# Optimization experiments

Measured on AMD Instinct MI355X. Metric: run time of the kernel, lower is better.

The kernel has to match this reference:

```python
import jax, jax.numpy as jnp
import numpy as np
from jax import lax

B, N, T, F, H, R = 32, 1024, 32, 5, 64, 5


def setup_inputs() -> dict:
    key = jax.random.key(0)
    ks = jax.random.split(key, 12)
    sc = 0.1
    x = jax.random.normal(ks[0], (B, N, T, F), dtype=jnp.float32)
    A = jax.random.randint(ks[1], (N, N, R), 0, 2).astype(jnp.float32)
    return {
        "x": x,
        "A": A,
        # nn.LSTM params (torch layout: [4H, in], gate order i,f,g,o)
        "lstm_Wih": jax.random.normal(ks[2], (4 * H, F), dtype=jnp.float32) * sc,
        "lstm_Whh": jax.random.normal(ks[3], (4 * H, H), dtype=jnp.float32) * sc,
        "lstm_bih": jax.random.normal(ks[4], (4 * H,), dtype=jnp.float32) * sc,
        "lstm_bhh": jax.random.normal(ks[5], (4 * H,), dtype=jnp.float32) * sc,
        # attention Linear(H, 1)
        "attn_w": jax.random.normal(ks[6], (1, H), dtype=jnp.float32) * sc,
        "attn_b": jax.random.normal(ks[7], (1,), dtype=jnp.float32) * sc,
        # GNN edge-gate Linear(R, 1)
        "gnn_w": jax.random.normal(ks[8], (1, R), dtype=jnp.float32) * sc,
        "gnn_b": jax.random.normal(ks[9], (1,), dtype=jnp.float32) * sc,
        # pred Linear(2H, 1)
        "pred_w": jax.random.normal(ks[10], (1, 2 * H), dtype=jnp.float32) * sc,
        "pred_b": jax.random.normal(ks[11], (1,), dtype=jnp.float32) * sc,
    }


def _lstm_attn(x, Wih, Whh, bih, bhh, attn_w, attn_b):
    # x: [BN, T, F] -> attended hidden [BN, H]
    BN, Tt, _ = x.shape
    Hh = Whh.shape[1]
    pre = x @ Wih.T + (bih + bhh)  # [BN, T, 4H] input projections precomputed

    def step(carry, xt):
        h, c = carry
        gates = xt + h @ Whh.T
        i, f, g, o = jnp.split(gates, 4, axis=-1)
        c = jax.nn.sigmoid(f) * c + jax.nn.sigmoid(i) * jnp.tanh(g)
        h = jax.nn.sigmoid(o) * jnp.tanh(c)
        return (h, c), h

    init = (jnp.zeros((BN, Hh), x.dtype), jnp.zeros((BN, Hh), x.dtype))
    _, hs = lax.scan(step, init, pre.transpose(1, 0, 2))
    hs = hs.transpose(1, 0, 2)  # [BN, T, H]
    scores = jnp.tanh(hs @ attn_w.T + attn_b)      # [BN, T, 1]
    aw = jax.nn.softmax(scores, axis=1)            # softmax over time
    return jnp.sum(hs * aw, axis=1)                # [BN, H]


def reference(x, A, lstm_Wih, lstm_Whh, lstm_bih, lstm_bhh,
              attn_w, attn_b, gnn_w, gnn_b, pred_w, pred_b):
    Bb, Nn, Tt, Ff = x.shape
    Hh = lstm_Whh.shape[1]
    # LSTM+attention shared across stocks -> fold stocks into batch
    e_old = _lstm_attn(x.reshape(Bb * Nn, Tt, Ff), lstm_Wih, lstm_Whh,
                       lstm_bih, lstm_bhh, attn_w, attn_b).reshape(Bb, Nn, Hh)

    # GNN: per-edge gate w[i,j] = LeakyReLU(Linear(A[i,j,:])), active if sum(A[i,j])>0
    mask = (jnp.sum(A, axis=-1) > 0).astype(e_old.dtype)             # [N, N]
    w = jax.nn.leaky_relu((A @ gnn_w.T + gnn_b)[..., 0], 0.2)        # [N, N]
    deg = jnp.sum(mask, axis=1)                                      # [N] active neighbor count
    coef = mask * w                                                  # [N, N]
    dots = jnp.einsum('bik,bjk->bij', e_old, e_old)                  # [B, N, N]
    e_new = jnp.einsum('bij,ij,bjk->bik', dots, coef, e_old) / deg[None, :, None]
    e_final = jnp.concatenate([e_old, e_new], axis=-1)               # [B, N, 2H]
    preds = e_final @ pred_w.T + pred_b                              # [B, N, 1]
    return preds
```

## Files before the change

### kernel.cpp

```cpp
#include <hip/hip_runtime.h>

constexpr int Bc = 32, Nc = 1024, Tc = 32, Fc = 5, Hc = 64;
constexpr int BNc = Bc * Nc;

#define DEVFN __device__ __forceinline__

typedef _Float16 f16x8 __attribute__((ext_vector_type(8)));
typedef _Float16 f16x4 __attribute__((ext_vector_type(4)));
typedef float    f32x16 __attribute__((ext_vector_type(16)));

DEVFN float fast_rcp(float x) { return __builtin_amdgcn_rcpf(x); }
DEVFN float tanh_fast(float x) { return 1.f - 2.f * fast_rcp(__expf(2.f * x) + 1.f); }

__global__ __launch_bounds__(128, 2) void lstm_attn_kernel(
    const float* __restrict__ x,
    const float* __restrict__ Wih,
    const float* __restrict__ Whh,
    const float* __restrict__ bih,
    const float* __restrict__ bhh,
    const float* __restrict__ attn_w,
    const float* __restrict__ attn_b,
    _Float16* __restrict__ E16,
    _Float16* __restrict__ ET)
{
    constexpr int XP = 164;
    constexpr int HP = 68;
    __shared__ __align__(16) _Float16 xs[32 * XP];
    __shared__ __align__(16) _Float16 hb[2][32 * HP];
    __shared__ float ap[2][32];
    float* es = (float*)xs;

    const int tid  = threadIdx.x;
    const int w    = tid >> 6;
    const int lane = tid & 63;
    const int m    = lane & 31;
    const int hi   = lane >> 5;

    const float* xg = x + (size_t)blockIdx.x * 32 * Tc * Fc;
    for (int i = tid; i < 32 * 160; i += 128) {
        int mm = i / 160, o = i - mm * 160;
        xs[mm * XP + o] = (_Float16)xg[i];
    }
    for (int i = tid; i < 32 * HP / 2; i += 128) ((uint*)&hb[0][0])[i] = 0u;

    f16x8 af[4][5];
    #pragma unroll
    for (int g = 0; g < 4; ++g) {
        const int j = 32 * (2 * g + w) + m;
        #pragma unroll
        for (int kt = 0; kt < 4; ++kt) {
            const float* wp = Whh + j * 64 + kt * 16 + 8 * hi;
            float4 u0 = *(const float4*)wp;
            float4 u1 = *(const float4*)(wp + 4);
            af[g][kt] = f16x8{(_Float16)u0.x, (_Float16)u0.y, (_Float16)u0.z, (_Float16)u0.w,
                              (_Float16)u1.x, (_Float16)u1.y, (_Float16)u1.z, (_Float16)u1.w};
        }
        float v[8];
        #pragma unroll
        for (int e = 0; e < 5; ++e) v[e] = Wih[j * Fc + e];
        v[5] = bih[j] + bhh[j]; v[6] = 0.f; v[7] = 0.f;
        #pragma unroll
        for (int e = 0; e < 8; ++e) {
            float z = hi ? 0.f : v[e];
            af[g][4][e] = (_Float16)z;
        }
    }

    float aw_own[16];
    #pragma unroll
    for (int a2 = 0; a2 < 4; ++a2)
        #pragma unroll
        for (int p = 0; p < 4; ++p)
            aw_own[a2 * 4 + p] = attn_w[32 * w + 8 * a2 + 4 * hi + p];
    const float ab = attn_b[0];

    float hcur[16], cst[16], oacc[16];
    #pragma unroll
    for (int i = 0; i < 16; ++i) { hcur[i] = 0.f; cst[i] = 0.f; oacc[i] = 0.f; }
    float lsum = 0.f;

    f32x16 zero16 = {0,0,0,0,0,0,0,0,0,0,0,0,0,0,0,0};
    const int xrow = m * XP;
    const int swz  = m & 15;
    __syncthreads();

    f16x8 bf[5];
    #pragma unroll
    for (int kt = 0; kt < 4; ++kt) {
        f16x4 lo = *(const f16x4*)&hb[0][m * HP + ((4 * kt + 2 * hi)     ^ swz) * 4];
        f16x4 hh = *(const f16x4*)&hb[0][m * HP + ((4 * kt + 2 * hi + 1) ^ swz) * 4];
        bf[kt] = f16x8{lo[0], lo[1], lo[2], lo[3], hh[0], hh[1], hh[2], hh[3]};
    }
    {
        #pragma unroll
        for (int e = 0; e < 8; ++e) bf[4][e] = (_Float16)0.f;
        if (!hi) {
            #pragma unroll
            for (int e = 0; e < 5; ++e) bf[4][e] = xs[xrow + e];
            bf[4][5] = (_Float16)1.f;
        }
    }

    #pragma unroll 1
    for (int t = 0; t < Tc; ++t) {
        f32x16 acc[4];
        #pragma unroll
        for (int g = 0; g < 4; ++g) {
            acc[g] = __builtin_amdgcn_mfma_f32_32x32x16_f16(af[g][0], bf[0], zero16, 0, 0, 0);
            #pragma unroll
            for (int kt = 1; kt < 5; ++kt)
                acc[g] = __builtin_amdgcn_mfma_f32_32x32x16_f16(af[g][kt], bf[kt], acc[g], 0, 0, 0);
        }
        float attnp = 0.f;
        #pragma unroll
        for (int r = 0; r < 16; ++r) {
            float ei = __expf(-acc[0][r]);
            float ef = __expf(-acc[1][r]);
            float Eg = __expf(2.f * acc[2][r]);
            float eo = __expf(-acc[3][r]);
            float u  = 1.f + ei;
            float v  = 1.f + ef;
            float wq = Eg + 1.f;
            float z  = Eg - 1.f;
            float t1 = u * wq;
            float num = fmaf(cst[r], t1, z * v);
            float cn = num * fast_rcp(t1 * v);
            cst[r] = cn;
            float E2 = __expf(2.f * cn);
            float hv = (E2 - 1.f) * fast_rcp((E2 + 1.f) * (1.f + eo));
            hcur[r] = hv;
            attnp = fmaf(hv, aw_own[r], attnp);
        }
        _Float16* hw = &hb[(t + 1) & 1][0];
        #pragma unroll
        for (int a2 = 0; a2 < 4; ++a2) {
            f16x4 pk = {(_Float16)hcur[4 * a2 + 0], (_Float16)hcur[4 * a2 + 1],
                        (_Float16)hcur[4 * a2 + 2], (_Float16)hcur[4 * a2 + 3]};
            *(f16x4*)&hw[m * HP + ((8 * w + 2 * a2 + hi) ^ swz) * 4] = pk;
        }
        attnp += __shfl_xor(attnp, 32);
        if (!hi) ap[w][m] = attnp;
        __syncthreads();
        float sc = tanh_fast(ap[0][m] + ap[1][m] + ab);
        float ew = __expf(sc);
        lsum += ew;
        #pragma unroll
        for (int i = 0; i < 16; ++i) oacc[i] = fmaf(ew, hcur[i], oacc[i]);
        if (t != Tc - 1) {
            const _Float16* hr = &hb[(t + 1) & 1][0];
            #pragma unroll
            for (int kt = 0; kt < 4; ++kt) {
                f16x4 lo = *(const f16x4*)&hr[m * HP + ((4 * kt + 2 * hi)     ^ swz) * 4];
                f16x4 hh = *(const f16x4*)&hr[m * HP + ((4 * kt + 2 * hi + 1) ^ swz) * 4];
                bf[kt] = f16x8{lo[0], lo[1], lo[2], lo[3], hh[0], hh[1], hh[2], hh[3]};
            }
            if (!hi) {
                #pragma unroll
                for (int e = 0; e < 5; ++e) bf[4][e] = xs[xrow + (t + 1) * Fc + e];
                bf[4][5] = (_Float16)1.f;
            }
        }
    }

    __syncthreads();
    const float li = fast_rcp(lsum);
    #pragma unroll
    for (int r = 0; r < 16; ++r) {
        int u = 32 * w + 8 * (r >> 2) + 4 * hi + (r & 3);
        es[m * 65 + u] = oacc[r] * li;
    }
    __syncthreads();

    uint* E16u = (uint*)E16 + (size_t)blockIdx.x * 32 * 32;
    for (int idx = tid; idx < 32 * 32; idx += 128) {
        int mm = idx >> 5, hp = idx & 31;
        union { _Float16 h2[2]; uint u; } cv;
        cv.h2[0] = (_Float16)es[mm * 65 + 2 * hp];
        cv.h2[1] = (_Float16)es[mm * 65 + 2 * hp + 1];
        E16u[idx] = cv.u;
    }
    const int bb_ = blockIdx.x >> 5, n0d = (blockIdx.x & 31) * 16;
    uint* ETu = (uint*)ET;
    for (int idx = tid; idx < 64 * 16; idx += 128) {
        int h = idx >> 4, c = idx & 15;
        union { _Float16 h2[2]; uint u; } cv;
        cv.h2[0] = (_Float16)es[(2 * c) * 65 + h];
        cv.h2[1] = (_Float16)es[(2 * c + 1) * 65 + h];
        ETu[((size_t)bb_ * 64 + h) * 512 + n0d + c] = cv.u;
    }
}

__global__ __launch_bounds__(256) void coefq_kernel(
    const float* __restrict__ A,
    const float* __restrict__ gnn_w,
    const float* __restrict__ gnn_b,
    float* __restrict__ coefQ,
    float* __restrict__ deg)
{
    __shared__ float ct[64 * 68];
    const int t = threadIdx.x;
    const int it = blockIdx.x >> 4, jt = blockIdx.x & 15;
    const int i_loc = t >> 2, chunk = t & 3;
    float gw[5];
    #pragma unroll
    for (int f = 0; f < 5; ++f) gw[f] = gnn_w[f];
    const float gb = gnn_b[0];

    const float* Ab = A + ((size_t)(it * 64 + i_loc) * 1024 + jt * 64 + chunk * 16) * 5;
    float buf[80];
    #pragma unroll
    for (int k = 0; k < 20; ++k)
        *(float4*)&buf[4 * k] = ((const float4*)Ab)[k];

    float cnt = 0.f;
    #pragma unroll
    for (int jj = 0; jj < 16; ++jj) {
        float s = 0.f, d = gb;
        #pragma unroll
        for (int f = 0; f < 5; ++f) { float vv = buf[5 * jj + f]; s += vv; d = fmaf(vv, gw[f], d); }
        float cf = (s > 0.f) ? (d >= 0.f ? d : 0.2f * d) : 0.f;
        ct[i_loc * 68 + chunk * 16 + jj] = cf;
        cnt += (s > 0.f) ? 1.f : 0.f;
    }
    cnt += __shfl_xor(cnt, 1);
    cnt += __shfl_xor(cnt, 2);
    if ((t & 3) == 0) atomicAdd(&deg[it * 64 + i_loc], cnt);
    __syncthreads();

    const int i_o = t & 63;
    #pragma unroll
    for (int p = 0; p < 4; ++p) {
        int jg = (t >> 6) + 4 * p;
        float4 v = *(const float4*)&ct[i_o * 68 + 4 * jg];
        ((float4*)coefQ)[(size_t)(jt * 16 + jg) * 1024 + it * 64 + i_o] = v;
    }
}

__global__ __launch_bounds__(256, 2) void gnn_pred_kernel(
    const _Float16* __restrict__ E16,
    const _Float16* __restrict__ ET,
    const float* __restrict__ coefQ,
    const float* __restrict__ deg,
    const float* __restrict__ pred_w,
    const float* __restrict__ pred_b,
    float* __restrict__ preds)
{
    __shared__ __align__(16) _Float16 tiles[2][4][64 * 64];
    const int tid  = threadIdx.x;
    const int w    = tid >> 6;
    const int lane = tid & 63;
    const int l31  = lane & 31;
    const int hi   = lane >> 5;
    const int it   = blockIdx.x >> 5;
    const int b    = blockIdx.x & 31;

    _Float16* EA = &tiles[0][w][0];
    _Float16* EB = &tiles[1][w][0];
    const float4* coefQ4 = (const float4*)coefQ;

    f16x8 eb[2][4];
    #pragma unroll
    for (int ni = 0; ni < 2; ++ni)
        #pragma unroll
        for (int kt = 0; kt < 4; ++kt)
            eb[ni][kt] = *(const f16x8*)(E16 +
                ((size_t)(b * 1024 + it * 64 + ni * 32 + l31) * 64 + 16 * kt + 8 * hi));

    f32x16 zero16 = {0,0,0,0,0,0,0,0,0,0,0,0,0,0,0,0};
    f32x16 oacc[2][2];
    #pragma unroll
    for (int mi = 0; mi < 2; ++mi)
        #pragma unroll
        for (int nh = 0; nh < 2; ++nh) oacc[mi][nh] = zero16;

    #pragma unroll 1
    for (int s = 0; s < 4; ++s) {
        const int jt = w * 4 + s;
        const _Float16* srcA = E16 + (size_t)(b * 1024 + jt * 64) * 64;
        const _Float16* srcB = ET + (size_t)b * 64 * 1024 + jt * 64;
        #pragma unroll
        for (int q = 0; q < 8; ++q) {
            int f = q * 64 + lane, r = f >> 3, c = f & 7;
            uint4 va = *(const uint4*)(srcA + r * 64 + c * 8);
            *(uint4*)(EA + r * 64 + ((c ^ (r & 7)) * 8)) = va;
            uint4 vb = *(const uint4*)(srcB + r * 1024 + c * 8);
            *(uint4*)(EB + r * 64 + ((c ^ (r & 7)) * 8)) = vb;
        }
        #pragma unroll 1
        for (int mj = 0; mj < 2; ++mj) {
            f16x8 af[4];
            #pragma unroll
            for (int kt = 0; kt < 4; ++kt)
                af[kt] = *(const f16x8*)(EA + (mj * 32 + l31) * 64 +
                                         (((2 * kt + hi) ^ (l31 & 7)) * 8));
            #pragma unroll
            for (int mi = 0; mi < 2; ++mi) {
                f32x16 a = __builtin_amdgcn_mfma_f32_32x32x16_f16(af[0], eb[mi][0], zero16, 0, 0, 0);
                #pragma unroll
                for (int kt = 1; kt < 4; ++kt)
                    a = __builtin_amdgcn_mfma_f32_32x32x16_f16(af[kt], eb[mi][kt], a, 0, 0, 0);
                #pragma unroll
                for (int rg = 0; rg < 4; ++rg) {
                    int j0 = jt * 64 + mj * 32 + 8 * rg + 4 * hi;
                    float4 cf = coefQ4[(size_t)(j0 >> 2) * 1024 + it * 64 + mi * 32 + l31];
                    a[4 * rg + 0] *= cf.x; a[4 * rg + 1] *= cf.y;
                    a[4 * rg + 2] *= cf.z; a[4 * rg + 3] *= cf.w;
                }
                f16x8 pa[2];
                #pragma unroll
                for (int kk = 0; kk < 2; ++kk) {
                    const int rg = 2 * kk;
                    #pragma unroll
                    for (int c4 = 0; c4 < 4; ++c4) {
                        float own_lo = a[rg * 4 + c4];
                        float own_hi = a[(rg + 1) * 4 + c4];
                        float send = hi ? own_lo : own_hi;
                        float recv = __shfl_xor(send, 32);
                        float lo = hi ? recv : own_lo;
                        float hv = hi ? own_hi : recv;
                        pa[kk][c4]     = (_Float16)lo;
                        pa[kk][4 + c4] = (_Float16)hv;
                    }
                }
                #pragma unroll
                for (int nh = 0; nh < 2; ++nh)
                    #pragma unroll
                    for (int kk = 0; kk < 2; ++kk) {
                        const int ktj = 2 * mj + kk;
                        f16x8 bb = *(const f16x8*)(EB + (nh * 32 + l31) * 64 +
                                                   (((2 * ktj + hi) ^ (l31 & 7)) * 8));
                        oacc[mi][nh] = __builtin_amdgcn_mfma_f32_32x32x16_f16(
                            pa[kk], bb, oacc[mi][nh], 0, 0, 0);
                    }
            }
        }
    }

    const float pwh0 = pred_w[64 + l31];
    const float pwh1 = pred_w[96 + l31];
    #pragma unroll
    for (int mi = 0; mi < 2; ++mi)
        #pragma unroll
        for (int r = 0; r < 16; ++r) {
            float v = oacc[mi][0][r] * pwh0 + oacc[mi][1][r] * pwh1;
            v += __shfl_xor(v, 1);  v += __shfl_xor(v, 2);  v += __shfl_xor(v, 4);
            v += __shfl_xor(v, 8);  v += __shfl_xor(v, 16);
            int i_loc = mi * 32 + 8 * (r >> 2) + (r & 3) + 4 * hi;
            int gi = it * 64 + i_loc;
            if (l31 == 0) {
                float dg = deg[gi];
                atomicAdd(&preds[b * 1024 + gi], v * fast_rcp(dg));
            }
        }
    if (w == 0) {
        const float pb0 = pred_b[0];
        #pragma unroll
        for (int ni = 0; ni < 2; ++ni) {
            float dot = 0.f;
            #pragma unroll
            for (int kt = 0; kt < 4; ++kt)
                #pragma unroll
                for (int e = 0; e < 8; ++e)
                    dot = fmaf((float)eb[ni][kt][e], pred_w[16 * kt + 8 * hi + e], dot);
            dot += __shfl_xor(dot, 32);
            if (hi == 0)
                atomicAdd(&preds[b * 1024 + it * 64 + ni * 32 + l31], dot + pb0);
        }
    }
}

extern "C" void kernel_launch(void* const* d_in, const int* in_sizes, int n_in,
                              void* d_out, int out_size, void* d_ws, size_t ws_size,
                              hipStream_t stream) {
    const float* x      = (const float*)d_in[0];
    const float* A      = (const float*)d_in[1];
    const float* Wih    = (const float*)d_in[2];
    const float* Whh    = (const float*)d_in[3];
    const float* bih    = (const float*)d_in[4];
    const float* bhh    = (const float*)d_in[5];
    const float* attn_w = (const float*)d_in[6];
    const float* attn_b = (const float*)d_in[7];
    const float* gnn_w  = (const float*)d_in[8];
    const float* gnn_b  = (const float*)d_in[9];
    const float* pred_w = (const float*)d_in[10];
    const float* pred_b = (const float*)d_in[11];
    float* preds = (float*)d_out;

    _Float16* E16 = (_Float16*)d_ws;
    _Float16* ET  = E16 + (size_t)BNc * Hc;
    float* coefQ  = (float*)(ET + (size_t)BNc * Hc);
    float* deg    = coefQ + (size_t)Nc * Nc;

    hipMemsetAsync(preds, 0, (size_t)out_size * sizeof(float), stream);
    hipMemsetAsync(deg, 0, Nc * sizeof(float), stream);

    lstm_attn_kernel<<<BNc / 32, 128, 0, stream>>>(x, Wih, Whh, bih, bhh,
                                                   attn_w, attn_b, E16, ET);
    coefq_kernel<<<256, 256, 0, stream>>>(A, gnn_w, gnn_b, coefQ, deg);
    gnn_pred_kernel<<<Bc * (Nc / 64), 256, 0, stream>>>(E16, ET, coefQ, deg,
                                                        pred_w, pred_b, preds);
}
```

Measured before the change: 237.3 us.

## Split LSTM gates across four waves and drop LDS staging in GNN kernel

The LSTM kernel now runs 256 threads per block, with each wave computing two interleaved gate tiles so a lane holds all four gates of a hidden unit. The h exchange uses a single 16-byte swizzled LDS write and read per step instead of split 8-byte accesses. The GNN kernel halves the row tile to 32, reads E16/ET directly from global memory instead of staging them in LDS, and reduces across waves in shared memory so it can write preds directly, removing the atomics and the memset. The goal is more parallelism and occupancy in the latency-bound recurrence, at the cost of more global loads in the GNN stage.

```diff
diff --git a/kernel.cpp b/kernel.cpp
--- a/kernel.cpp
+++ b/kernel.cpp
@@ -6,13 +6,12 @@
 #define DEVFN __device__ __forceinline__
 
 typedef _Float16 f16x8 __attribute__((ext_vector_type(8)));
-typedef _Float16 f16x4 __attribute__((ext_vector_type(4)));
 typedef float    f32x16 __attribute__((ext_vector_type(16)));
 
 DEVFN float fast_rcp(float x) { return __builtin_amdgcn_rcpf(x); }
 DEVFN float tanh_fast(float x) { return 1.f - 2.f * fast_rcp(__expf(2.f * x) + 1.f); }
 
-__global__ __launch_bounds__(128, 2) void lstm_attn_kernel(
+__global__ __launch_bounds__(256, 3) void lstm_attn_kernel(
     const float* __restrict__ x,
     const float* __restrict__ Wih,
     const float* __restrict__ Whh,
@@ -24,10 +23,9 @@
     _Float16* __restrict__ ET)
 {
     constexpr int XP = 164;
-    constexpr int HP = 68;
     __shared__ __align__(16) _Float16 xs[32 * XP];
-    __shared__ __align__(16) _Float16 hb[2][32 * HP];
-    __shared__ float ap[2][32];
+    __shared__ __align__(16) _Float16 hb[2][32 * 64];
+    __shared__ float ap[4][32];
     float* es = (float*)xs;
 
     const int tid  = threadIdx.x;
@@ -37,23 +35,23 @@
     const int hi   = lane >> 5;
 
     const float* xg = x + (size_t)blockIdx.x * 32 * Tc * Fc;
-    for (int i = tid; i < 32 * 160; i += 128) {
+    for (int i = tid; i < 32 * 160; i += 256) {
         int mm = i / 160, o = i - mm * 160;
         xs[mm * XP + o] = (_Float16)xg[i];
     }
-    for (int i = tid; i < 32 * HP / 2; i += 128) ((uint*)&hb[0][0])[i] = 0u;
-
-    f16x8 af[4][5];
-    #pragma unroll
-    for (int g = 0; g < 4; ++g) {
-        const int j = 32 * (2 * g + w) + m;
+
+    f16x8 af[2][5];
+    #pragma unroll
+    for (int tt = 0; tt < 2; ++tt) {
+        const int jt = 2 * w + tt;
+        const int j  = 64 * (m & 3) + 8 * jt + (m >> 2);
         #pragma unroll
         for (int kt = 0; kt < 4; ++kt) {
             const float* wp = Whh + j * 64 + kt * 16 + 8 * hi;
             float4 u0 = *(const float4*)wp;
             float4 u1 = *(const float4*)(wp + 4);
-            af[g][kt] = f16x8{(_Float16)u0.x, (_Float16)u0.y, (_Float16)u0.z, (_Float16)u0.w,
-                              (_Float16)u1.x, (_Float16)u1.y, (_Float16)u1.z, (_Float16)u1.w};
+            af[tt][kt] = f16x8{(_Float16)u0.x, (_Float16)u0.y, (_Float16)u0.z, (_Float16)u0.w,
+                               (_Float16)u1.x, (_Float16)u1.y, (_Float16)u1.z, (_Float16)u1.w};
         }
         float v[8];
         #pragma unroll
@@ -62,98 +60,102 @@
         #pragma unroll
         for (int e = 0; e < 8; ++e) {
             float z = hi ? 0.f : v[e];
-            af[g][4][e] = (_Float16)z;
-        }
-    }
-
-    float aw_own[16];
-    #pragma unroll
-    for (int a2 = 0; a2 < 4; ++a2)
-        #pragma unroll
-        for (int p = 0; p < 4; ++p)
-            aw_own[a2 * 4 + p] = attn_w[32 * w + 8 * a2 + 4 * hi + p];
+            af[tt][4][e] = (_Float16)z;
+        }
+    }
+
+    float aw_own[8];
+    #pragma unroll
+    for (int tt = 0; tt < 2; ++tt)
+        #pragma unroll
+        for (int a = 0; a < 4; ++a)
+            aw_own[tt * 4 + a] = attn_w[16 * w + 8 * tt + 2 * a + hi];
     const float ab = attn_b[0];
 
-    float hcur[16], cst[16], oacc[16];
-    #pragma unroll
-    for (int i = 0; i < 16; ++i) { hcur[i] = 0.f; cst[i] = 0.f; oacc[i] = 0.f; }
+    float hcur[8], cst[8], oacc[8];
+    #pragma unroll
+    for (int i = 0; i < 8; ++i) { hcur[i] = 0.f; cst[i] = 0.f; oacc[i] = 0.f; }
     float lsum = 0.f;
 
     f32x16 zero16 = {0,0,0,0,0,0,0,0,0,0,0,0,0,0,0,0};
     const int xrow = m * XP;
-    const int swz  = m & 15;
+    const int sw8  = m & 7;
     __syncthreads();
 
     f16x8 bf[5];
     #pragma unroll
-    for (int kt = 0; kt < 4; ++kt) {
-        f16x4 lo = *(const f16x4*)&hb[0][m * HP + ((4 * kt + 2 * hi)     ^ swz) * 4];
-        f16x4 hh = *(const f16x4*)&hb[0][m * HP + ((4 * kt + 2 * hi + 1) ^ swz) * 4];
-        bf[kt] = f16x8{lo[0], lo[1], lo[2], lo[3], hh[0], hh[1], hh[2], hh[3]};
-    }
-    {
-        #pragma unroll
-        for (int e = 0; e < 8; ++e) bf[4][e] = (_Float16)0.f;
-        if (!hi) {
-            #pragma unroll
-            for (int e = 0; e < 5; ++e) bf[4][e] = xs[xrow + e];
-            bf[4][5] = (_Float16)1.f;
-        }
+    for (int kt = 0; kt < 4; ++kt)
+        #pragma unroll
+        for (int e = 0; e < 8; ++e) bf[kt][e] = (_Float16)0.f;
+    #pragma unroll
+    for (int e = 0; e < 8; ++e) bf[4][e] = (_Float16)0.f;
+    if (!hi) {
+        #pragma unroll
+        for (int e = 0; e < 5; ++e) bf[4][e] = xs[xrow + e];
+        bf[4][5] = (_Float16)1.f;
     }
 
     #pragma unroll 1
     for (int t = 0; t < Tc; ++t) {
-        f32x16 acc[4];
-        #pragma unroll
-        for (int g = 0; g < 4; ++g) {
-            acc[g] = __builtin_amdgcn_mfma_f32_32x32x16_f16(af[g][0], bf[0], zero16, 0, 0, 0);
+        f32x16 acc[2];
+        #pragma unroll
+        for (int tt = 0; tt < 2; ++tt) {
+            acc[tt] = __builtin_amdgcn_mfma_f32_32x32x16_f16(af[tt][0], bf[0], zero16, 0, 0, 0);
             #pragma unroll
             for (int kt = 1; kt < 5; ++kt)
-                acc[g] = __builtin_amdgcn_mfma_f32_32x32x16_f16(af[g][kt], bf[kt], acc[g], 0, 0, 0);
+                acc[tt] = __builtin_amdgcn_mfma_f32_32x32x16_f16(af[tt][kt], bf[kt], acc[tt], 0, 0, 0);
         }
         float attnp = 0.f;
         #pragma unroll
-        for (int r = 0; r < 16; ++r) {
-            float ei = __expf(-acc[0][r]);
-            float ef = __expf(-acc[1][r]);
-            float Eg = __expf(2.f * acc[2][r]);
-            float eo = __expf(-acc[3][r]);
-            float u  = 1.f + ei;
-            float v  = 1.f + ef;
-            float wq = Eg + 1.f;
-            float z  = Eg - 1.f;
-            float t1 = u * wq;
-            float num = fmaf(cst[r], t1, z * v);
-            float cn = num * fast_rcp(t1 * v);
-            cst[r] = cn;
-            float E2 = __expf(2.f * cn);
-            float hv = (E2 - 1.f) * fast_rcp((E2 + 1.f) * (1.f + eo));
-            hcur[r] = hv;
-            attnp = fmaf(hv, aw_own[r], attnp);
-        }
-        _Float16* hw = &hb[(t + 1) & 1][0];
-        #pragma unroll
-        for (int a2 = 0; a2 < 4; ++a2) {
-            f16x4 pk = {(_Float16)hcur[4 * a2 + 0], (_Float16)hcur[4 * a2 + 1],
-                        (_Float16)hcur[4 * a2 + 2], (_Float16)hcur[4 * a2 + 3]};
-            *(f16x4*)&hw[m * HP + ((8 * w + 2 * a2 + hi) ^ swz) * 4] = pk;
+        for (int tt = 0; tt < 2; ++tt)
+            #pragma unroll
+            for (int a = 0; a < 4; ++a) {
+                const int ci = tt * 4 + a;
+                float ei = __expf(-acc[tt][4 * a + 0]);
+                float ef = __expf(-acc[tt][4 * a + 1]);
+                float Eg = __expf(2.f * acc[tt][4 * a + 2]);
+                float eo = __expf(-acc[tt][4 * a + 3]);
+                float u  = 1.f + ei;
+                float v  = 1.f + ef;
+                float wq = Eg + 1.f;
+                float z  = Eg - 1.f;
+                float t1 = u * wq;
+                float num = fmaf(cst[ci], t1, z * v);
+                float cn = num * fast_rcp(t1 * v);
+                cst[ci] = cn;
+                float E2 = __expf(2.f * cn);
+                float hv = (E2 - 1.f) * fast_rcp((E2 + 1.f) * (1.f + eo));
+                hcur[ci] = hv;
+                attnp = fmaf(hv, aw_own[ci], attnp);
+            }
+        {
+            float recv[4];
+            #pragma unroll
+            for (int a = 0; a < 4; ++a) {
+                float send = hcur[(hi ? 0 : 1) * 4 + a];
+                recv[a] = __shfl_xor(send, 32);
+            }
+            f16x8 pk;
+            #pragma unroll
+            for (int a = 0; a < 4; ++a) {
+                pk[2 * a]     = (_Float16)(hi ? recv[a]      : hcur[a]);
+                pk[2 * a + 1] = (_Float16)(hi ? hcur[4 + a]  : recv[a]);
+            }
+            *(f16x8*)&hb[t & 1][m * 64 + (((2 * w + hi) ^ sw8) * 8)] = pk;
         }
         attnp += __shfl_xor(attnp, 32);
         if (!hi) ap[w][m] = attnp;
         __syncthreads();
-        float sc = tanh_fast(ap[0][m] + ap[1][m] + ab);
+        float sc = tanh_fast(ap[0][m] + ap[1][m] + ap[2][m] + ap[3][m] + ab);
         float ew = __expf(sc);
         lsum += ew;
         #pragma unroll
-        for (int i = 0; i < 16; ++i) oacc[i] = fmaf(ew, hcur[i], oacc[i]);
+        for (int i = 0; i < 8; ++i) oacc[i] = fmaf(ew, hcur[i], oacc[i]);
         if (t != Tc - 1) {
-            const _Float16* hr = &hb[(t + 1) & 1][0];
-            #pragma unroll
-            for (int kt = 0; kt < 4; ++kt) {
-                f16x4 lo = *(const f16x4*)&hr[m * HP + ((4 * kt + 2 * hi)     ^ swz) * 4];
-                f16x4 hh = *(const f16x4*)&hr[m * HP + ((4 * kt + 2 * hi + 1) ^ swz) * 4];
-                bf[kt] = f16x8{lo[0], lo[1], lo[2], lo[3], hh[0], hh[1], hh[2], hh[3]};
-            }
+            const _Float16* hr = &hb[t & 1][0];
+            #pragma unroll
+            for (int kt = 0; kt < 4; ++kt)
+                bf[kt] = *(const f16x8*)&hr[m * 64 + (((2 * kt + hi) ^ sw8) * 8)];
             if (!hi) {
                 #pragma unroll
                 for (int e = 0; e < 5; ++e) bf[4][e] = xs[xrow + (t + 1) * Fc + e];
@@ -165,14 +167,16 @@
     __syncthreads();
     const float li = fast_rcp(lsum);
     #pragma unroll
-    for (int r = 0; r < 16; ++r) {
-        int u = 32 * w + 8 * (r >> 2) + 4 * hi + (r & 3);
-        es[m * 65 + u] = oacc[r] * li;
-    }
+    for (int tt = 0; tt < 2; ++tt)
+        #pragma unroll
+        for (int a = 0; a < 4; ++a) {
+            int u = 16 * w + 8 * tt + 2 * a + hi;
+            es[m * 65 + u] = oacc[tt * 4 + a] * li;
+        }
     __syncthreads();
 
     uint* E16u = (uint*)E16 + (size_t)blockIdx.x * 32 * 32;
-    for (int idx = tid; idx < 32 * 32; idx += 128) {
+    for (int idx = tid; idx < 32 * 32; idx += 256) {
         int mm = idx >> 5, hp = idx & 31;
         union { _Float16 h2[2]; uint u; } cv;
         cv.h2[0] = (_Float16)es[mm * 65 + 2 * hp];
@@ -181,7 +185,7 @@
     }
     const int bb_ = blockIdx.x >> 5, n0d = (blockIdx.x & 31) * 16;
     uint* ETu = (uint*)ET;
-    for (int idx = tid; idx < 64 * 16; idx += 128) {
+    for (int idx = tid; idx < 64 * 16; idx += 256) {
         int h = idx >> 4, c = idx & 15;
         union { _Float16 h2[2]; uint u; } cv;
         cv.h2[0] = (_Float16)es[(2 * c) * 65 + h];
@@ -236,7 +240,7 @@
     }
 }
 
-__global__ __launch_bounds__(256, 2) void gnn_pred_kernel(
+__global__ __launch_bounds__(256, 3) void gnn_pred_kernel(
     const _Float16* __restrict__ E16,
     const _Float16* __restrict__ ET,
     const float* __restrict__ coefQ,
@@ -245,7 +249,7 @@
     const float* __restrict__ pred_b,
     float* __restrict__ preds)
 {
-    __shared__ __align__(16) _Float16 tiles[2][4][64 * 64];
+    __shared__ float pacc[4][32];
     const int tid  = threadIdx.x;
     const int w    = tid >> 6;
     const int lane = tid & 63;
@@ -254,117 +258,91 @@
     const int it   = blockIdx.x >> 5;
     const int b    = blockIdx.x & 31;
 
-    _Float16* EA = &tiles[0][w][0];
-    _Float16* EB = &tiles[1][w][0];
     const float4* coefQ4 = (const float4*)coefQ;
 
-    f16x8 eb[2][4];
-    #pragma unroll
-    for (int ni = 0; ni < 2; ++ni)
-        #pragma unroll
-        for (int kt = 0; kt < 4; ++kt)
-            eb[ni][kt] = *(const f16x8*)(E16 +
-                ((size_t)(b * 1024 + it * 64 + ni * 32 + l31) * 64 + 16 * kt + 8 * hi));
+    f16x8 eb[4];
+    #pragma unroll
+    for (int kt = 0; kt < 4; ++kt)
+        eb[kt] = *(const f16x8*)(E16 +
+            (size_t)(b * 1024 + it * 32 + l31) * 64 + kt * 16 + 8 * hi);
 
     f32x16 zero16 = {0,0,0,0,0,0,0,0,0,0,0,0,0,0,0,0};
-    f32x16 oacc[2][2];
-    #pragma unroll
-    for (int mi = 0; mi < 2; ++mi)
-        #pragma unroll
-        for (int nh = 0; nh < 2; ++nh) oacc[mi][nh] = zero16;
+    f32x16 oacc[2] = {zero16, zero16};
 
     #pragma unroll 1
     for (int s = 0; s < 4; ++s) {
-        const int jt = w * 4 + s;
-        const _Float16* srcA = E16 + (size_t)(b * 1024 + jt * 64) * 64;
-        const _Float16* srcB = ET + (size_t)b * 64 * 1024 + jt * 64;
-        #pragma unroll
-        for (int q = 0; q < 8; ++q) {
-            int f = q * 64 + lane, r = f >> 3, c = f & 7;
-            uint4 va = *(const uint4*)(srcA + r * 64 + c * 8);
-            *(uint4*)(EA + r * 64 + ((c ^ (r & 7)) * 8)) = va;
-            uint4 vb = *(const uint4*)(srcB + r * 1024 + c * 8);
-            *(uint4*)(EB + r * 64 + ((c ^ (r & 7)) * 8)) = vb;
-        }
+        const int jt = 4 * w + s;
         #pragma unroll 1
         for (int mj = 0; mj < 2; ++mj) {
-            f16x8 af[4];
+            f16x8 afr[4];
             #pragma unroll
             for (int kt = 0; kt < 4; ++kt)
-                af[kt] = *(const f16x8*)(EA + (mj * 32 + l31) * 64 +
-                                         (((2 * kt + hi) ^ (l31 & 7)) * 8));
-            #pragma unroll
-            for (int mi = 0; mi < 2; ++mi) {
-                f32x16 a = __builtin_amdgcn_mfma_f32_32x32x16_f16(af[0], eb[mi][0], zero16, 0, 0, 0);
+                afr[kt] = *(const f16x8*)(E16 +
+                    (size_t)(b * 1024 + jt * 64 + mj * 32 + l31) * 64 + kt * 16 + 8 * hi);
+            f32x16 a = __builtin_amdgcn_mfma_f32_32x32x16_f16(afr[0], eb[0], zero16, 0, 0, 0);
+            #pragma unroll
+            for (int kt = 1; kt < 4; ++kt)
+                a = __builtin_amdgcn_mfma_f32_32x32x16_f16(afr[kt], eb[kt], a, 0, 0, 0);
+            #pragma unroll
+            for (int rg = 0; rg < 4; ++rg) {
+                int j0 = jt * 64 + mj * 32 + 8 * rg + 4 * hi;
+                float4 cf = coefQ4[(size_t)(j0 >> 2) * 1024 + it * 32 + l31];
+                a[4 * rg + 0] *= cf.x; a[4 * rg + 1] *= cf.y;
+                a[4 * rg + 2] *= cf.z; a[4 * rg + 3] *= cf.w;
+            }
+            f16x8 pa[2];
+            #pragma unroll
+            for (int kk = 0; kk < 2; ++kk) {
+                const int rg = 2 * kk;
                 #pragma unroll
-                for (int kt = 1; kt < 4; ++kt)
-                    a = __builtin_amdgcn_mfma_f32_32x32x16_f16(af[kt], eb[mi][kt], a, 0, 0, 0);
-                #pragma unroll
-                for (int rg = 0; rg < 4; ++rg) {
-                    int j0 = jt * 64 + mj * 32 + 8 * rg + 4 * hi;
-                    float4 cf = coefQ4[(size_t)(j0 >> 2) * 1024 + it * 64 + mi * 32 + l31];
-                    a[4 * rg + 0] *= cf.x; a[4 * rg + 1] *= cf.y;
-                    a[4 * rg + 2] *= cf.z; a[4 * rg + 3] *= cf.w;
+                for (int c4 = 0; c4 < 4; ++c4) {
+                    float own_lo = a[rg * 4 + c4];
+                    float own_hi = a[(rg + 1) * 4 + c4];
+                    float send = hi ? own_lo : own_hi;
+                    float recv = __shfl_xor(send, 32);
+                    float lo = hi ? recv : own_lo;
+                    float hv = hi ? own_hi : recv;
+                    pa[kk][c4]     = (_Float16)lo;
+                    pa[kk][4 + c4] = (_Float16)hv;
                 }
-                f16x8 pa[2];
+            }
+            #pragma unroll
+            for (int nh = 0; nh < 2; ++nh)
                 #pragma unroll
                 for (int kk = 0; kk < 2; ++kk) {
-                    const int rg = 2 * kk;
-                    #pragma unroll
-                    for (int c4 = 0; c4 < 4; ++c4) {
-                        float own_lo = a[rg * 4 + c4];
-                        float own_hi = a[(rg + 1) * 4 + c4];
-                        float send = hi ? own_lo : own_hi;
-                        float recv = __shfl_xor(send, 32);
-                        float lo = hi ? recv : own_lo;
-                        float hv = hi ? own_hi : recv;
-                        pa[kk][c4]     = (_Float16)lo;
-                        pa[kk][4 + c4] = (_Float16)hv;
-                    }
+                    const int ktj = 2 * mj + kk;
+                    f16x8 bb = *(const f16x8*)(ET +
+                        (size_t)(b * 64 + nh * 32 + l31) * 1024 +
+                        jt * 64 + ktj * 16 + 8 * hi);
+                    oacc[nh] = __builtin_amdgcn_mfma_f32_32x32x16_f16(
+                        pa[kk], bb, oacc[nh], 0, 0, 0);
                 }
-                #pragma unroll
-                for (int nh = 0; nh < 2; ++nh)
-                    #pragma unroll
-                    for (int kk = 0; kk < 2; ++kk) {
-                        const int ktj = 2 * mj + kk;
-                        f16x8 bb = *(const f16x8*)(EB + (nh * 32 + l31) * 64 +
-                                                   (((2 * ktj + hi) ^ (l31 & 7)) * 8));
-                        oacc[mi][nh] = __builtin_amdgcn_mfma_f32_32x32x16_f16(
-                            pa[kk], bb, oacc[mi][nh], 0, 0, 0);
-                    }
-            }
         }
     }
 
     const float pwh0 = pred_w[64 + l31];
     const float pwh1 = pred_w[96 + l31];
     #pragma unroll
-    for (int mi = 0; mi < 2; ++mi)
-        #pragma unroll
-        for (int r = 0; r < 16; ++r) {
-            float v = oacc[mi][0][r] * pwh0 + oacc[mi][1][r] * pwh1;
-            v += __shfl_xor(v, 1);  v += __shfl_xor(v, 2);  v += __shfl_xor(v, 4);
-            v += __shfl_xor(v, 8);  v += __shfl_xor(v, 16);
-            int i_loc = mi * 32 + 8 * (r >> 2) + (r & 3) + 4 * hi;
-            int gi = it * 64 + i_loc;
-            if (l31 == 0) {
-                float dg = deg[gi];
-                atomicAdd(&preds[b * 1024 + gi], v * fast_rcp(dg));
-            }
-        }
+    for (int r = 0; r < 16; ++r) {
+        float v = oacc[0][r] * pwh0 + oacc[1][r] * pwh1;
+        v += __shfl_xor(v, 1);  v += __shfl_xor(v, 2);  v += __shfl_xor(v, 4);
+        v += __shfl_xor(v, 8);  v += __shfl_xor(v, 16);
+        int i_loc = 8 * (r >> 2) + (r & 3) + 4 * hi;
+        if (l31 == 0) pacc[w][i_loc] = v;
+    }
+    __syncthreads();
     if (w == 0) {
-        const float pb0 = pred_b[0];
-        #pragma unroll
-        for (int ni = 0; ni < 2; ++ni) {
-            float dot = 0.f;
-            #pragma unroll
-            for (int kt = 0; kt < 4; ++kt)
-                #pragma unroll
-                for (int e = 0; e < 8; ++e)
-                    dot = fmaf((float)eb[ni][kt][e], pred_w[16 * kt + 8 * hi + e], dot);
-            dot += __shfl_xor(dot, 32);
-            if (hi == 0)
-                atomicAdd(&preds[b * 1024 + it * 64 + ni * 32 + l31], dot + pb0);
+        float dot = 0.f;
+        #pragma unroll
+        for (int kt = 0; kt < 4; ++kt)
+            #pragma unroll
+            for (int e = 0; e < 8; ++e)
+                dot = fmaf((float)eb[kt][e], pred_w[16 * kt + 8 * hi + e], dot);
+        dot += __shfl_xor(dot, 32);
+        if (hi == 0) {
+            int gi = it * 32 + l31;
+            float osum = pacc[0][l31] + pacc[1][l31] + pacc[2][l31] + pacc[3][l31];
+            preds[b * 1024 + gi] = dot + osum * fast_rcp(deg[gi]) + pred_b[0];
         }
     }
 }
@@ -391,12 +369,11 @@
     float* coefQ  = (float*)(ET + (size_t)BNc * Hc);
     float* deg    = coefQ + (size_t)Nc * Nc;
 
-    hipMemsetAsync(preds, 0, (size_t)out_size * sizeof(float), stream);
     hipMemsetAsync(deg, 0, Nc * sizeof(float), stream);
 
-    lstm_attn_kernel<<<BNc / 32, 128, 0, stream>>>(x, Wih, Whh, bih, bhh,
+    lstm_attn_kernel<<<BNc / 32, 256, 0, stream>>>(x, Wih, Whh, bih, bhh,
                                                    attn_w, attn_b, E16, ET);
     coefq_kernel<<<256, 256, 0, stream>>>(A, gnn_w, gnn_b, coefQ, deg);
-    gnn_pred_kernel<<<Bc * (Nc / 64), 256, 0, stream>>>(E16, ET, coefQ, deg,
+    gnn_pred_kernel<<<Bc * (Nc / 32), 256, 0, stream>>>(E16, ET, coefQ, deg,
                                                         pred_w, pred_b, preds);
 }
```

Measured after the change: 253.3 us. +6.7%, slower.
